# Optimization experiments

Hardware: AMD Instinct MI355X
Metric: run time of the kernel (lower is better)

## Reference

```python
import jax, jax.numpy as jnp
import numpy as np

EDGES = [(5, 7), (7, 9), (6, 8), (8, 10), (5, 6), (5, 11), (6, 12), (11, 12),
         (11, 13), (13, 15), (12, 14), (14, 16), (0, 5), (0, 6)]
N_NODES = 17

def _build_norm_adj():
    # aggregated[dst] += h[src] for both directions; then divide by clamped in-degree.
    A = np.zeros((N_NODES, N_NODES), dtype=np.float32)
    for s, d in EDGES:
        A[d, s] += 1.0
        A[s, d] += 1.0
    deg = np.clip(A.sum(axis=1, keepdims=True), 1.0, None)
    return jnp.asarray(A / deg)  # (17, 17)

_A_NORM = _build_norm_adj()

def _bn17(x, gamma, beta, eps=1e-5):
    # BatchNorm1d(17) on (B, 17, D): stats over batch and feature dims per node channel.
    mean = x.mean(axis=(0, 2), keepdims=True)
    var = x.var(axis=(0, 2), keepdims=True)  # biased, matching torch training mode
    return gamma[None, :, None] * (x - mean) * jax.lax.rsqrt(var + eps) + beta[None, :, None]

def setup_inputs() -> dict:
    key = jax.random.key(0)
    ks = jax.random.split(key, 8)
    B, H, E = 65536, 64, 128
    s = 0.1
    return {
        "x": jax.random.normal(ks[0], (B, N_NODES, 2), jnp.float32),
        "W_enc": jax.random.normal(ks[1], (2, H), jnp.float32) * s,
        "b_enc": jnp.zeros((H,), jnp.float32),
        "W_gc1": jax.random.normal(ks[2], (H, H), jnp.float32) * s,
        "b_gc1": jnp.zeros((H,), jnp.float32),
        "W_gc2": jax.random.normal(ks[3], (H, H), jnp.float32) * s,
        "b_gc2": jnp.zeros((H,), jnp.float32),
        "gamma1": jnp.ones((N_NODES,), jnp.float32),
        "beta1": jnp.zeros((N_NODES,), jnp.float32),
        "gamma2": jnp.ones((N_NODES,), jnp.float32),
        "beta2": jnp.zeros((N_NODES,), jnp.float32),
        "W_p1": jax.random.normal(ks[4], (N_NODES * H, 256), jnp.float32) * s,
        "b_p1": jnp.zeros((256,), jnp.float32),
        "W_p2": jax.random.normal(ks[5], (256, E), jnp.float32) * s,
        "b_p2": jnp.zeros((E,), jnp.float32),
    }

def reference(x, W_enc, b_enc, W_gc1, b_gc1, W_gc2, b_gc2,
              gamma1, beta1, gamma2, beta2, W_p1, b_p1, W_p2, b_p2):
    B = x.shape[0]
    # node encoder (dropout = identity at inference)
    h = jax.nn.relu(jnp.einsum('bnc,cd->bnd', x, W_enc) + b_enc)
    # graph conv 1: normalized neighbor mean via fixed adjacency
    h_agg = jnp.einsum('ij,bjd->bid', _A_NORM, h)
    h = _bn17(h + h_agg, gamma1, beta1)
    h = jax.nn.relu(jnp.einsum('bnd,de->bne', h, W_gc1) + b_gc1)
    # graph conv 2
    h_agg = jnp.einsum('ij,bjd->bid', _A_NORM, h)
    h = _bn17(h + h_agg, gamma2, beta2)
    h = jax.nn.relu(jnp.einsum('bnd,de->bne', h, W_gc2) + b_gc2)
    # pool MLP (dropout = identity)
    pooled = h.reshape(B, -1)  # (B, 17*64)
    z = jax.nn.relu(pooled @ W_p1 + b_p1)
    emb = z @ W_p2 + b_p2
    # L2 normalize (torch F.normalize eps=1e-12)
    norm = jnp.sqrt(jnp.sum(emb * emb, axis=1, keepdims=True))
    return emb / jnp.maximum(norm, 1e-12)
```

## Files before the change

kernel.cpp:

```cpp
#include <hip/hip_runtime.h>
#include <hip/hip_bf16.h>

typedef unsigned int  uint32;
typedef unsigned short ushort16;

#define B_TOTAL 65536
#define NN 17

typedef __bf16 bf16x8 __attribute__((ext_vector_type(8)));
typedef float  f32x4  __attribute__((ext_vector_type(4)));

static constexpr int   CNT[NN]    = {2,0,0,0,0,4,4,2,2,1,1,3,3,2,2,1,1};
static constexpr int   NBR[NN][4] = {
  {5,6,0,0},{0,0,0,0},{0,0,0,0},{0,0,0,0},{0,0,0,0},
  {7,6,11,0},{8,5,12,0},{5,9,0,0},{6,10,0,0},{7,0,0,0},{8,0,0,0},
  {5,12,13,0},{6,11,14,0},{11,15,0,0},{12,16,0,0},{13,0,0,0},{14,0,0,0}};
static constexpr float INVDEG[NN] = {0.5f,0.f,0.f,0.f,0.f,0.25f,0.25f,0.5f,0.5f,1.f,1.f,
  0.33333333333333333f,0.33333333333333333f,0.5f,0.5f,1.f,1.f};

#define S_BYTES   ((size_t)B_TOTAL * 1088 * 2)
#define STATS_OFF S_BYTES
#define W1_OFF    (STATS_OFF + 40960)
#define W2_OFF    (W1_OFF + (size_t)278528*2)
#define WGT_OFF   (W2_OFF + (size_t)65536)


__device__ inline ushort16 f2bfu(float f){
  union { __hip_bfloat16 h; ushort16 u; } c; c.h = __float2bfloat16(f); return c.u;
}

__device__ inline f32x4 MFMA(bf16x8 a, bf16x8 b, f32x4 c){
  return __builtin_amdgcn_mfma_f32_16x16x32_bf16(a, b, c, 0, 0, 0);
}

__device__ inline void enc_agg(const float* __restrict__ xb,
                               float we0, float we1, float be, float* s1){
  float h[NN];
  #pragma unroll
  for (int n = 0; n < NN; ++n)
    h[n] = fmaxf(fmaf(xb[2*n], we0, fmaf(xb[2*n+1], we1, be)), 0.f);
  #pragma unroll
  for (int n = 0; n < NN; ++n){
    float a = 0.f;
    #pragma unroll
    for (int j = 0; j < 4; ++j) if (j < CNT[n]) a += h[NBR[n][j]];
    s1[n] = fmaf(INVDEG[n], a, h[n]);
  }
}

__device__ inline void reduce_stats(float* sA, float* qA,
                                    float* __restrict__ gSum, float* __restrict__ gSq){
  int t = threadIdx.x;
  #pragma unroll
  for (int n = 0; n < NN; ++n){
    float s = sA[n], q = qA[n];
    #pragma unroll
    for (int off = 32; off > 0; off >>= 1){
      s += __shfl_down(s, off, 64);
      q += __shfl_down(q, off, 64);
    }
    sA[n] = s; qA[n] = q;
  }
  __shared__ float shS[NN], shQ[NN];
  if (t < NN){ shS[t] = 0.f; shQ[t] = 0.f; }
  __syncthreads();
  if ((t & 63) == 0){
    #pragma unroll
    for (int n = 0; n < NN; ++n){ atomicAdd(&shS[n], sA[n]); atomicAdd(&shQ[n], qA[n]); }
  }
  __syncthreads();
  if (t < NN){ atomicAdd(&gSum[t], shS[t]); atomicAdd(&gSq[t], shQ[t]); }
}

__device__ inline void mfma_stats(const char* hsm, float* sred, int t,
                                  float* __restrict__ gSum, float* __restrict__ gSq){
  const int w4 = t >> 6, lo = t & 15, q = (t >> 4) & 3;
  bf16x8 one;
  { union { ushort16 u[8]; bf16x8 v; } c;
    #pragma unroll
    for (int i = 0; i < 8; ++i) c.u[i] = 0x3F80;
    one = c.v; }
  #pragma unroll
  for (int i = 0; i < 5; ++i){
    int mt = w4 + i*4;
    if (mt < 17){
      f32x4 d0 = (f32x4)0.f, d1 = (f32x4)0.f;
      #pragma unroll
      for (int s = 0; s < 2; ++s){
        int r = mt*16 + lo;
        bf16x8 a = *(const bf16x8*)(hsm + ((r*128 + s*64 + q*16) ^ ((r & 7) << 4)));
        d0 = MFMA(a, one, d0);
        d1 = MFMA(a, a, d1);
      }
      if (lo == 0){
        #pragma unroll
        for (int j = 0; j < 4; ++j) sred[mt*16 + q*4 + j] = d0[j];
      }
      if ((lo >> 2) == q) sred[272 + mt*16 + lo] = d1[lo & 3];
    }
  }
  __syncthreads();
  if (t < NN){
    float s = 0.f, qq = 0.f;
    #pragma unroll
    for (int bl = 0; bl < 16; ++bl){
      s  += sred[t + 17*bl];
      qq += sred[272 + t + 17*bl];
    }
    atomicAdd(&gSum[t], s);
    atomicAdd(&gSq[t], qq);
  }
}

__global__ __launch_bounds__(256) void k_prep(const float* __restrict__ Wp1,
                                              const float* __restrict__ Wp2,
                                              const float* __restrict__ Wg1,
                                              const float* __restrict__ Wg2,
                                              ushort16* __restrict__ W1T,
                                              ushort16* __restrict__ W2T,
                                              ushort16* __restrict__ WGT,
                                              float* __restrict__ colsum2){
  int g = blockIdx.x * 256 + threadIdx.x;
  if (g < 278528){
    int n = g / 1088, k = g - n*1088;
    W1T[g] = f2bfu(Wp1[(size_t)k*256 + n]);
  } else if (g < 311296){
    int h = g - 278528;
    int e = h >> 8, k = h & 255;
    W2T[h] = f2bfu(Wp2[(size_t)k*128 + e]);
  } else if (g < 327680){
    int h = g - 311296;
    int sel = h >> 12;
    int idx = h & 4095;
    int e = idx >> 6, d = idx & 63;
    const float* Wsrc = (sel < 2) ? Wg1 : Wg2;
    float v = Wsrc[d*64 + e];
    __hip_bfloat16 hi = __float2bfloat16(v);
    if (sel & 1){
      float rem = v - __bfloat162float(hi);
      WGT[h] = f2bfu(rem);
    } else {
      WGT[h] = f2bfu(v);
    }
  } else {
    int e = g - 327680;
    if (e < 64){
      float cs = 0.f;
      for (int d = 0; d < 64; ++d){
        float v = Wg2[d*64 + e];
        float hi = __bfloat162float(__float2bfloat16(v));
        float lo = __bfloat162float(__float2bfloat16(v - hi));
        cs += hi + lo;
      }
      colsum2[e] = cs;
    }
  }
}

__global__ void k_sh(const float* __restrict__ shift2, const float* __restrict__ colsum2,
                     const float* __restrict__ bg2, float* __restrict__ SH){
  int n = blockIdx.x, e = threadIdx.x;
  SH[n*64 + e] = fmaf(shift2[n], colsum2[e], bg2[e]);
}

__global__ __launch_bounds__(256,4) void k_stats1(const float* __restrict__ x,
    const float* __restrict__ W_enc, const float* __restrict__ b_enc,
    float* __restrict__ gSum, float* __restrict__ gSq){
  __shared__ __align__(16) float xs[1088];
  int t = threadIdx.x, e = t & 63, lb = t >> 6;
  float we0 = W_enc[e], we1 = W_enc[64 + e], be = b_enc[e];
  const float4* xg = (const float4*)(x + (size_t)blockIdx.x*1088);
  ((float4*)xs)[t] = xg[t];
  if (t < 16) ((float4*)xs)[256 + t] = xg[256 + t];
  float sA[NN], qA[NN];
  #pragma unroll
  for (int n = 0; n < NN; ++n){ sA[n] = 0.f; qA[n] = 0.f; }
  __syncthreads();
  for (int it = 0; it < 8; ++it){
    float s1[NN];
    enc_agg(xs + (it*4 + lb)*34, we0, we1, be, s1);
    #pragma unroll
    for (int n = 0; n < NN; ++n){ sA[n] += s1[n]; qA[n] += s1[n]*s1[n]; }
  }
  int slot = (blockIdx.x & 31) * 32;
  reduce_stats(sA, qA, gSum + slot, gSq + slot);
}

__global__ void k_finalize(const float* __restrict__ gSum, const float* __restrict__ gSq,
                           const float* __restrict__ gamma, const float* __restrict__ beta,
                           float* __restrict__ scale, float* __restrict__ shift){
  int n = threadIdx.x;
  if (n < NN){
    float s = 0.f, qq = 0.f;
    for (int sl = 0; sl < 32; ++sl){ s += gSum[sl*32 + n]; qq += gSq[sl*32 + n]; }
    const float invC = 1.0f / (float)((size_t)B_TOTAL * 64);
    float mean = s * invC;
    float var  = qq * invC - mean*mean;
    float istd = rsqrtf(var + 1e-5f);
    float sc   = gamma[n] * istd;
    scale[n] = sc;
    shift[n] = fmaf(-mean, sc, beta[n]);
  }
}

__global__ __launch_bounds__(256,4) void k_gc1(const float* __restrict__ x,
    const float* __restrict__ W_enc, const float* __restrict__ b_enc,
    const float* __restrict__ bg,
    const float* __restrict__ scale, const float* __restrict__ shift,
    const __hip_bfloat16* __restrict__ Whi, const __hip_bfloat16* __restrict__ Wlo,
    __hip_bfloat16* __restrict__ S, float* __restrict__ gSum, float* __restrict__ gSq){
  __shared__ __align__(16) char hsm[272*128];
  __shared__ float sred[544];
  __shared__ __align__(16) float xs[544];
  __shared__ float sc_s[NN], sf_s[NN];
  const int t = threadIdx.x, e = t & 63, lb = t >> 6;
  const int w4 = t >> 6, lo = t & 15, q = (t >> 4) & 3;
  if (t < NN){ sc_s[t] = scale[t]; sf_s[t] = shift[t]; }
  if (t < 136) ((float4*)xs)[t] = ((const float4*)(x + (size_t)blockIdx.x*544))[t];
  float we0 = W_enc[e], we1 = W_enc[64 + e], be = b_enc[e];
  __syncthreads();

  for (int it = 0; it < 4; ++it){
    int bl = it*4 + lb;
    float s1[NN];
    enc_agg(xs + bl*34, we0, we1, be, s1);
    #pragma unroll
    for (int n = 0; n < NN; ++n){
      int row = bl*17 + n;
      int byt = (row*128 + 2*e) ^ ((row & 7) << 4);
      *(__hip_bfloat16*)(hsm + byt) = __float2bfloat16(fmaf(s1[n], sc_s[n], sf_s[n]));
    }
  }
  __syncthreads();

  const char* WhiB = (const char*)Whi;
  const char* WloB = (const char*)Wlo;
  f32x4 acc[5][4];
  #pragma unroll
  for (int i = 0; i < 5; ++i)
    #pragma unroll
    for (int et = 0; et < 4; ++et) acc[i][et] = (f32x4)0.f;
  #pragma unroll
  for (int et = 0; et < 4; ++et){
    int col = et*16 + lo;
    bf16x8 wh0 = *(const bf16x8*)(WhiB + col*128 +      q*16);
    bf16x8 wh1 = *(const bf16x8*)(WhiB + col*128 + 64 + q*16);
    bf16x8 wl0 = *(const bf16x8*)(WloB + col*128 +      q*16);
    bf16x8 wl1 = *(const bf16x8*)(WloB + col*128 + 64 + q*16);
    #pragma unroll
    for (int i = 0; i < 5; ++i){
      int mt = w4 + i*4;
      if (mt < 17){
        int r = mt*16 + lo;
        int base = r*128, sw = (r & 7) << 4;
        bf16x8 a0 = *(const bf16x8*)(hsm + ((base +      q*16) ^ sw));
        bf16x8 a1 = *(const bf16x8*)(hsm + ((base + 64 + q*16) ^ sw));
        acc[i][et] = MFMA(a0, wh0, acc[i][et]);
        acc[i][et] = MFMA(a1, wh1, acc[i][et]);
        acc[i][et] = MFMA(a0, wl0, acc[i][et]);
        acc[i][et] = MFMA(a1, wl1, acc[i][et]);
      }
    }
  }
  float bgv[4];
  #pragma unroll
  for (int et = 0; et < 4; ++et) bgv[et] = bg[et*16 + lo];
  __syncthreads();

  #pragma unroll
  for (int i = 0; i < 5; ++i){
    int mt = w4 + i*4;
    if (mt < 17){
      #pragma unroll
      for (int et = 0; et < 4; ++et){
        #pragma unroll
        for (int j = 0; j < 4; ++j){
          int row = mt*16 + q*4 + j;
          float h2 = fmaxf(acc[i][et][j] + bgv[et], 0.f);
          int byt = (row*128 + (et*16 + lo)*2) ^ ((row & 7) << 4);
          *(__hip_bfloat16*)(hsm + byt) = __float2bfloat16(h2);
        }
      }
    }
  }
  __syncthreads();

  for (int it = 0; it < 4; ++it){
    int bl = it*4 + lb;
    int row0 = bl*17;
    float h2v[NN];
    #pragma unroll
    for (int n = 0; n < NN; ++n){
      int row = row0 + n;
      h2v[n] = __bfloat162float(*(const __hip_bfloat16*)(hsm + ((row*128 + 2*e) ^ ((row & 7) << 4))));
    }
    #pragma unroll
    for (int n = 0; n < NN; ++n){
      float agg = 0.f;
      #pragma unroll
      for (int j = 0; j < 4; ++j) if (j < CNT[n]) agg += h2v[NBR[n][j]];
      float s2 = fmaf(INVDEG[n], agg, h2v[n]);
      int row = row0 + n;
      *(__hip_bfloat16*)(hsm + ((row*128 + 2*e) ^ ((row & 7) << 4))) = __float2bfloat16(s2);
    }
  }
  __syncthreads();

  int slot = (blockIdx.x & 31) * 32;
  mfma_stats(hsm, sred, t, gSum + slot, gSq + slot);

  const size_t gbase = (size_t)blockIdx.x * 34816;
  char* Sc = (char*)S;
  #pragma unroll
  for (int k = 0; k < 9; ++k){
    int g = t + k*256;
    if (g < 2176){
      int row = g >> 3;
      uint4 v = *(const uint4*)(hsm + ((g*16) ^ ((row & 7) << 4)));
      *(uint4*)(Sc + gbase + (size_t)g*16) = v;
    }
  }
}

__global__ __launch_bounds__(256,2) void k_back(
    const __hip_bfloat16* __restrict__ S,
    const ushort16* __restrict__ W1T, const float* __restrict__ b_p1,
    const ushort16* __restrict__ W2T, const float* __restrict__ b_p2,
    const __hip_bfloat16* __restrict__ WG2,
    const float* __restrict__ scale2, const float* __restrict__ SH,
    float* __restrict__ out){
  __shared__ __align__(16) char smem[65536];
  const int t = threadIdx.x;
  const int L = t & 63, w = t >> 6;
  const int lo = L & 15, q = L >> 4;
  const size_t b0 = (size_t)blockIdx.x * 128;
  const char* Sb  = (const char*)S;
  const char* W1b = (const char*)W1T;
  const char* W2b = (const char*)W2T;
  const char* Wgb = (const char*)WG2;

  f32x4 acc[16][2];
  #pragma unroll
  for (int nt = 0; nt < 16; ++nt){ acc[nt][0] = (f32x4)0.f; acc[nt][1] = (f32x4)0.f; }

  uint4 wr0, wr1, wr2, wr3;
  auto loadW = [&](int ks){
    size_t kb = (size_t)ks * 64;
    wr0 = *(const uint4*)(W1b + (size_t)((  0 + t) >> 2)*2176 + kb + (t&3)*16);
    wr1 = *(const uint4*)(W1b + (size_t)((256 + t) >> 2)*2176 + kb + (t&3)*16);
    wr2 = *(const uint4*)(W1b + (size_t)((512 + t) >> 2)*2176 + kb + (t&3)*16);
    wr3 = *(const uint4*)(W1b + (size_t)((768 + t) >> 2)*2176 + kb + (t&3)*16);
  };
  auto writeW = [&](int buf){
    char* Wb = smem + 32768 + (buf ? 16384 : 0);
    *(uint4*)(Wb + (size_t)t*16)          = wr0;
    *(uint4*)(Wb + (size_t)(256 + t)*16)  = wr1;
    *(uint4*)(Wb + (size_t)(512 + t)*16)  = wr2;
    *(uint4*)(Wb + (size_t)(768 + t)*16)  = wr3;
  };

  uint4 br[4];
  auto loadS2 = [&](int n){
    const char* base = Sb + (b0 + (size_t)(w*32 + lo))*2176 + n*128 + q*16;
    br[0] = *(const uint4*)(base);
    br[1] = *(const uint4*)(base + 64);
    br[2] = *(const uint4*)(base + 16*2176);
    br[3] = *(const uint4*)(base + 16*2176 + 64);
  };
  auto gc2w = [&](int n){
    char* Pb = smem + (n & 1)*16384;
    float sc = scale2[n];
    f32x4 g[2][4];
    #pragma unroll
    for (int bt = 0; bt < 2; ++bt)
      #pragma unroll
      for (int et = 0; et < 4; ++et) g[bt][et] = (f32x4)0.f;
    #pragma unroll
    for (int et = 0; et < 4; ++et){
      const char* A = Wgb + (et*16 + lo)*128 + q*16;
      bf16x8 ah0 = *(const bf16x8*)(A);
      bf16x8 ah1 = *(const bf16x8*)(A + 64);
      bf16x8 al0 = *(const bf16x8*)(A + 8192);
      bf16x8 al1 = *(const bf16x8*)(A + 8192 + 64);
      #pragma unroll
      for (int bt = 0; bt < 2; ++bt){
        union { uint4 u; bf16x8 v; } c0, c1;
        c0.u = br[bt*2]; c1.u = br[bt*2 + 1];
        g[bt][et] = MFMA(ah0, c0.v, g[bt][et]);
        g[bt][et] = MFMA(al0, c0.v, g[bt][et]);
        g[bt][et] = MFMA(ah1, c1.v, g[bt][et]);
        g[bt][et] = MFMA(al1, c1.v, g[bt][et]);
      }
    }
    #pragma unroll
    for (int et = 0; et < 4; ++et){
      float4 sh4 = *(const float4*)&SH[n*64 + et*16 + q*4];
      #pragma unroll
      for (int bt = 0; bt < 2; ++bt){
        int b = w*32 + bt*16 + lo;
        float v0 = fmaxf(fmaf(sc, g[bt][et].x, sh4.x), 0.f);
        float v1 = fmaxf(fmaf(sc, g[bt][et].y, sh4.y), 0.f);
        float v2 = fmaxf(fmaf(sc, g[bt][et].z, sh4.z), 0.f);
        float v3 = fmaxf(fmaf(sc, g[bt][et].w, sh4.w), 0.f);
        uint32 u0 = (uint32)f2bfu(v0) | ((uint32)f2bfu(v1) << 16);
        uint32 u1 = (uint32)f2bfu(v2) | ((uint32)f2bfu(v3) << 16);
        int byt = (b*128 + (et*16 + q*4)*2) ^ ((b & 7) << 4);
        *(uint2*)(Pb + byt) = make_uint2(u0, u1);
      }
    }
  };

  loadW(0);
  loadS2(0);
  gc2w(0);
  writeW(0);
  __syncthreads();

  #pragma unroll 1
  for (int ks = 0; ks < 34; ++ks){
    const int cur = ks & 1, n = ks >> 1, half = ks & 1;
    if (ks < 33) loadW(ks + 1);
    if (half == 0 && n < 16) loadS2(n + 1);
    const char* Pb = smem + (n & 1)*16384;
    const char* Wb = smem + 32768 + (cur ? 16384 : 0);
    int r0 = w*32 + lo, r1 = w*32 + 16 + lo;
    bf16x8 pf0 = *(const bf16x8*)(Pb + ((r0*128 + half*64 + q*16) ^ ((r0 & 7) << 4)));
    bf16x8 pf1 = *(const bf16x8*)(Pb + ((r1*128 + half*64 + q*16) ^ ((r1 & 7) << 4)));
    #pragma unroll
    for (int nt = 0; nt < 16; ++nt){
      bf16x8 wf = *(const bf16x8*)(Wb + (nt*16 + lo)*64 + q*16);
      acc[nt][0] = MFMA(wf, pf0, acc[nt][0]);
      acc[nt][1] = MFMA(wf, pf1, acc[nt][1]);
    }
    if (half == 1 && n < 16) gc2w(n + 1);
    if (ks < 33) writeW(cur ^ 1);
    __syncthreads();
  }

  #pragma unroll
  for (int nt = 0; nt < 16; ++nt){
    float4 bias = *(const float4*)&b_p1[nt*16 + q*4];
    #pragma unroll
    for (int bt = 0; bt < 2; ++bt){
      int b = w*32 + bt*16 + lo;
      f32x4 v = acc[nt][bt];
      float z0 = fmaxf(v.x + bias.x, 0.f), z1 = fmaxf(v.y + bias.y, 0.f);
      float z2 = fmaxf(v.z + bias.z, 0.f), z3 = fmaxf(v.w + bias.w, 0.f);
      uint32 lo32 = (uint32)f2bfu(z0) | ((uint32)f2bfu(z1) << 16);
      uint32 hi32 = (uint32)f2bfu(z2) | ((uint32)f2bfu(z3) << 16);
      int nbyte = (nt*16 + q*4) * 2;
      int addr = b*512 + (nbyte ^ ((b & 7) << 4));
      *(uint2*)(smem + addr) = make_uint2(lo32, hi32);
    }
  }
  __syncthreads();

  f32x4 acc2[8][2];
  #pragma unroll
  for (int et = 0; et < 8; ++et){ acc2[et][0] = (f32x4)0.f; acc2[et][1] = (f32x4)0.f; }
  #pragma unroll 1
  for (int ks = 0; ks < 8; ++ks){
    bf16x8 zf0, zf1;
    {
      int b = w*32 + lo;
      int kb = ks*64 + q*16;
      zf0 = *(const bf16x8*)(smem + b*512 + (kb ^ ((b & 7) << 4)));
      b = w*32 + 16 + lo;
      zf1 = *(const bf16x8*)(smem + b*512 + (kb ^ ((b & 7) << 4)));
    }
    #pragma unroll
    for (int et = 0; et < 8; ++et){
      bf16x8 wf = *(const bf16x8*)(W2b + (et*16 + lo)*512 + ks*64 + q*16);
      acc2[et][0] = MFMA(wf, zf0, acc2[et][0]);
      acc2[et][1] = MFMA(wf, zf1, acc2[et][1]);
    }
  }

  #pragma unroll
  for (int bt = 0; bt < 2; ++bt){
    int b = w*32 + bt*16 + lo;
    float4 vv[8];
    float ss = 0.f;
    #pragma unroll
    for (int et = 0; et < 8; ++et){
      float4 bias = *(const float4*)&b_p2[et*16 + q*4];
      f32x4 a = bt ? acc2[et][1] : acc2[et][0];
      vv[et].x = a.x + bias.x; vv[et].y = a.y + bias.y;
      vv[et].z = a.z + bias.z; vv[et].w = a.w + bias.w;
      ss += vv[et].x*vv[et].x + vv[et].y*vv[et].y + vv[et].z*vv[et].z + vv[et].w*vv[et].w;
    }
    ss += __shfl_xor(ss, 16, 64);
    ss += __shfl_xor(ss, 32, 64);
    float inv = 1.0f / fmaxf(sqrtf(ss), 1e-12f);
    float* op = out + (b0 + b)*128;
    #pragma unroll
    for (int et = 0; et < 8; ++et){
      float4 o; o.x = vv[et].x*inv; o.y = vv[et].y*inv; o.z = vv[et].z*inv; o.w = vv[et].w*inv;
      *(float4*)(op + et*16 + q*4) = o;
    }
  }
}

extern "C" void kernel_launch(void* const* d_in, const int* in_sizes, int n_in,
                              void* d_out, int out_size, void* d_ws, size_t ws_size,
                              hipStream_t stream) {
  const float* x     = (const float*)d_in[0];
  const float* W_enc = (const float*)d_in[1];
  const float* b_enc = (const float*)d_in[2];
  const float* W_gc1 = (const float*)d_in[3];
  const float* b_gc1 = (const float*)d_in[4];
  const float* W_gc2 = (const float*)d_in[5];
  const float* b_gc2 = (const float*)d_in[6];
  const float* gamma1= (const float*)d_in[7];
  const float* beta1 = (const float*)d_in[8];
  const float* gamma2= (const float*)d_in[9];
  const float* beta2 = (const float*)d_in[10];
  const float* W_p1  = (const float*)d_in[11];
  const float* b_p1  = (const float*)d_in[12];
  const float* W_p2  = (const float*)d_in[13];
  const float* b_p2  = (const float*)d_in[14];
  float* out = (float*)d_out;

  char* ws = (char*)d_ws;
  __hip_bfloat16* S = (__hip_bfloat16*)ws;
  float*    stats = (float*)(ws + STATS_OFF);
  ushort16* W1T   = (ushort16*)(ws + W1_OFF);
  ushort16* W2T   = (ushort16*)(ws + W2_OFF);
  __hip_bfloat16* WGT = (__hip_bfloat16*)(ws + WGT_OFF);

  (void)hipMemsetAsync(stats, 0, 16384, stream);

  k_prep<<<1281, 256, 0, stream>>>(W_p1, W_p2, W_gc1, W_gc2, W1T, W2T,
                                   (ushort16*)WGT, stats + 4224);
  k_stats1<<<2048, 256, 0, stream>>>(x, W_enc, b_enc, stats + 0, stats + 1024);
  k_finalize<<<1, 32, 0, stream>>>(stats + 0, stats + 1024, gamma1, beta1,
                                   stats + 4096, stats + 4128);
  k_gc1<<<4096, 256, 0, stream>>>(x, W_enc, b_enc, b_gc1,
                                  stats + 4096, stats + 4128,
                                  WGT, WGT + 4096,
                                  S, stats + 2048, stats + 3072);
  k_finalize<<<1, 32, 0, stream>>>(stats + 2048, stats + 3072, gamma2, beta2,
                                   stats + 4160, stats + 4192);
  k_sh<<<17, 64, 0, stream>>>(stats + 4192, stats + 4224, b_gc2, stats + 4288);
  k_back<<<512, 256, 0, stream>>>(S, W1T, b_p1, W2T, b_p2,
                                  WGT + 8192, stats + 4160, stats + 4288, out);
}
```

Measured before the change: 330.9 us.

## Stage pool weights via direct global-to-LDS loads and hoist graph-conv weights

Replaces the register round-trip for staging W_p1 tiles (global load into VGPRs, then an LDS store) with `global_load_lds` 16-byte transfers that write straight into the double-buffered LDS tile. It also loads the WG2 (graph-conv 2) MFMA fragments once into registers before the main loop, rather than re-reading them from global memory on every gc2w call. gc2w is reordered per batch tile so fewer accumulators are live at once. The aim is to cut VGPR pressure, LDS-store instructions and repeated weight fetches, at the cost of 64 extra persistent registers. It also relies on the barrier waiting for the asynchronous LDS writes to complete.

After: 324.3 us (median of 3 runs). -2.0%, faster.

```diff
diff --git a/kernel.cpp b/kernel.cpp
--- a/kernel.cpp
+++ b/kernel.cpp
@@ -31,6 +31,12 @@
 
 __device__ inline f32x4 MFMA(bf16x8 a, bf16x8 b, f32x4 c){
   return __builtin_amdgcn_mfma_f32_16x16x32_bf16(a, b, c, 0, 0, 0);
+}
+
+__device__ inline void gload_lds16(const void* g, void* l){
+  __builtin_amdgcn_global_load_lds(
+      (const __attribute__((address_space(1))) unsigned int*)g,
+      (__attribute__((address_space(3))) unsigned int*)l, 16, 0, 0);
 }
 
 __device__ inline void enc_agg(const float* __restrict__ xb,
@@ -343,20 +349,23 @@
   #pragma unroll
   for (int nt = 0; nt < 16; ++nt){ acc[nt][0] = (f32x4)0.f; acc[nt][1] = (f32x4)0.f; }
 
-  uint4 wr0, wr1, wr2, wr3;
-  auto loadW = [&](int ks){
+  bf16x8 wg[4][4];
+  #pragma unroll
+  for (int et = 0; et < 4; ++et){
+    const char* A = Wgb + (et*16 + lo)*128 + q*16;
+    wg[et][0] = *(const bf16x8*)(A);
+    wg[et][1] = *(const bf16x8*)(A + 64);
+    wg[et][2] = *(const bf16x8*)(A + 8192);
+    wg[et][3] = *(const bf16x8*)(A + 8192 + 64);
+  }
+
+  auto stageW = [&](int ks, int buf){
     size_t kb = (size_t)ks * 64;
-    wr0 = *(const uint4*)(W1b + (size_t)((  0 + t) >> 2)*2176 + kb + (t&3)*16);
-    wr1 = *(const uint4*)(W1b + (size_t)((256 + t) >> 2)*2176 + kb + (t&3)*16);
-    wr2 = *(const uint4*)(W1b + (size_t)((512 + t) >> 2)*2176 + kb + (t&3)*16);
-    wr3 = *(const uint4*)(W1b + (size_t)((768 + t) >> 2)*2176 + kb + (t&3)*16);
-  };
-  auto writeW = [&](int buf){
-    char* Wb = smem + 32768 + (buf ? 16384 : 0);
-    *(uint4*)(Wb + (size_t)t*16)          = wr0;
-    *(uint4*)(Wb + (size_t)(256 + t)*16)  = wr1;
-    *(uint4*)(Wb + (size_t)(512 + t)*16)  = wr2;
-    *(uint4*)(Wb + (size_t)(768 + t)*16)  = wr3;
+    char* ldsbase = smem + 32768 + buf*16384 + w*1024;
+    gload_lds16(W1b + (size_t)((  0 + t) >> 2)*2176 + kb + (t&3)*16, ldsbase);
+    gload_lds16(W1b + (size_t)((256 + t) >> 2)*2176 + kb + (t&3)*16, ldsbase + 4096);
+    gload_lds16(W1b + (size_t)((512 + t) >> 2)*2176 + kb + (t&3)*16, ldsbase + 8192);
+    gload_lds16(W1b + (size_t)((768 + t) >> 2)*2176 + kb + (t&3)*16, ldsbase + 12288);
   };
 
   uint4 br[4];
@@ -370,38 +379,28 @@
   auto gc2w = [&](int n){
     char* Pb = smem + (n & 1)*16384;
     float sc = scale2[n];
-    f32x4 g[2][4];
-    #pragma unroll
-    for (int bt = 0; bt < 2; ++bt)
+    #pragma unroll
+    for (int bt = 0; bt < 2; ++bt){
+      f32x4 g[4];
       #pragma unroll
-      for (int et = 0; et < 4; ++et) g[bt][et] = (f32x4)0.f;
-    #pragma unroll
-    for (int et = 0; et < 4; ++et){
-      const char* A = Wgb + (et*16 + lo)*128 + q*16;
-      bf16x8 ah0 = *(const bf16x8*)(A);
-      bf16x8 ah1 = *(const bf16x8*)(A + 64);
-      bf16x8 al0 = *(const bf16x8*)(A + 8192);
-      bf16x8 al1 = *(const bf16x8*)(A + 8192 + 64);
+      for (int et = 0; et < 4; ++et) g[et] = (f32x4)0.f;
+      union { uint4 u; bf16x8 v; } c0, c1;
+      c0.u = br[bt*2]; c1.u = br[bt*2 + 1];
       #pragma unroll
-      for (int bt = 0; bt < 2; ++bt){
-        union { uint4 u; bf16x8 v; } c0, c1;
-        c0.u = br[bt*2]; c1.u = br[bt*2 + 1];
-        g[bt][et] = MFMA(ah0, c0.v, g[bt][et]);
-        g[bt][et] = MFMA(al0, c0.v, g[bt][et]);
-        g[bt][et] = MFMA(ah1, c1.v, g[bt][et]);
-        g[bt][et] = MFMA(al1, c1.v, g[bt][et]);
-      }
-    }
-    #pragma unroll
-    for (int et = 0; et < 4; ++et){
-      float4 sh4 = *(const float4*)&SH[n*64 + et*16 + q*4];
+      for (int et = 0; et < 4; ++et){
+        g[et] = MFMA(wg[et][0], c0.v, g[et]);
+        g[et] = MFMA(wg[et][2], c0.v, g[et]);
+        g[et] = MFMA(wg[et][1], c1.v, g[et]);
+        g[et] = MFMA(wg[et][3], c1.v, g[et]);
+      }
+      int b = w*32 + bt*16 + lo;
       #pragma unroll
-      for (int bt = 0; bt < 2; ++bt){
-        int b = w*32 + bt*16 + lo;
-        float v0 = fmaxf(fmaf(sc, g[bt][et].x, sh4.x), 0.f);
-        float v1 = fmaxf(fmaf(sc, g[bt][et].y, sh4.y), 0.f);
-        float v2 = fmaxf(fmaf(sc, g[bt][et].z, sh4.z), 0.f);
-        float v3 = fmaxf(fmaf(sc, g[bt][et].w, sh4.w), 0.f);
+      for (int et = 0; et < 4; ++et){
+        float4 sh4 = *(const float4*)&SH[n*64 + et*16 + q*4];
+        float v0 = fmaxf(fmaf(sc, g[et].x, sh4.x), 0.f);
+        float v1 = fmaxf(fmaf(sc, g[et].y, sh4.y), 0.f);
+        float v2 = fmaxf(fmaf(sc, g[et].z, sh4.z), 0.f);
+        float v3 = fmaxf(fmaf(sc, g[et].w, sh4.w), 0.f);
         uint32 u0 = (uint32)f2bfu(v0) | ((uint32)f2bfu(v1) << 16);
         uint32 u1 = (uint32)f2bfu(v2) | ((uint32)f2bfu(v3) << 16);
         int byt = (b*128 + (et*16 + q*4)*2) ^ ((b & 7) << 4);
@@ -410,16 +409,15 @@
     }
   };
 
-  loadW(0);
   loadS2(0);
   gc2w(0);
-  writeW(0);
+  stageW(0, 0);
   __syncthreads();
 
   #pragma unroll 1
   for (int ks = 0; ks < 34; ++ks){
     const int cur = ks & 1, n = ks >> 1, half = ks & 1;
-    if (ks < 33) loadW(ks + 1);
+    if (ks < 33) stageW(ks + 1, cur ^ 1);
     if (half == 0 && n < 16) loadS2(n + 1);
     const char* Pb = smem + (n & 1)*16384;
     const char* Wb = smem + 32768 + (cur ? 16384 : 0);
@@ -433,7 +431,6 @@
       acc[nt][1] = MFMA(wf, pf1, acc[nt][1]);
     }
     if (half == 1 && n < 16) gc2w(n + 1);
-    if (ks < 33) writeW(cur ^ 1);
     __syncthreads();
   }
 
```
